# Performance work log

Measured on AMD Instinct MI355X. Metric: run time of the kernel, lower is better.

## Reference

```python
import jax, jax.numpy as jnp
import numpy as np

VOCAB, DIM, LAYERS, HEADS, FF, SEQ, BATCH = 32000, 1024, 4, 16, 4096, 2048, 2
HD = DIM // HEADS
EPS = 1e-6
ROPE_BASE = 10000.0


def setup_inputs() -> dict:
    key = jax.random.key(0)
    ks = jax.random.split(key, 10)
    std = 0.02
    return {
        "input_ids": jax.random.randint(ks[0], (BATCH, SEQ), 0, VOCAB, dtype=jnp.int32),
        "emb": jax.random.normal(ks[1], (VOCAB, DIM), jnp.float32) * std,
        "qkv_w": jax.random.normal(ks[2], (LAYERS, 3 * DIM, DIM), jnp.float32) * std,
        "out_w": jax.random.normal(ks[3], (LAYERS, DIM, DIM), jnp.float32) * std,
        "fc1_w": jax.random.normal(ks[4], (LAYERS, FF, DIM), jnp.float32) * std,
        "fc2_w": jax.random.normal(ks[5], (LAYERS, DIM, FF), jnp.float32) * std,
        "norm1_s": jnp.ones((LAYERS, DIM), jnp.float32),
        "norm2_s": jnp.ones((LAYERS, DIM), jnp.float32),
        "normf_s": jnp.ones((DIM,), jnp.float32),
        "lm_w": jax.random.normal(ks[6], (VOCAB, DIM), jnp.float32) * std,
    }


def _rms(x, scale):
    return x * jax.lax.rsqrt(jnp.mean(x * x, axis=-1, keepdims=True) + EPS) * scale


def _rope_tables(seq_len):
    inv_freq = 1.0 / (ROPE_BASE ** (jnp.arange(0, HD, 2, dtype=jnp.float32) / HD))
    freqs = jnp.arange(seq_len, dtype=jnp.float32)[:, None] * inv_freq[None, :]  # [S, HD/2]
    emb = jnp.concatenate([freqs, freqs], axis=-1)  # [S, HD]
    return jnp.cos(emb), jnp.sin(emb)


def _rotate_half(x):
    x1, x2 = jnp.split(x, 2, axis=-1)
    return jnp.concatenate([-x2, x1], axis=-1)


def _attention(h, qkv_w, out_w, cos, sin, mask):
    B, S, _ = h.shape
    qkv = jnp.einsum('bsd,ed->bse', h, qkv_w)  # [B, S, 3*DIM]
    qkv = qkv.reshape(B, S, 3, HEADS, HD).transpose(2, 0, 3, 1, 4)  # [3, B, H, S, hd]
    q, k, v = qkv[0], qkv[1], qkv[2]
    q = q * cos + _rotate_half(q) * sin
    k = k * cos + _rotate_half(k) * sin
    scores = jnp.einsum('bhqd,bhkd->bhqk', q, k) * (HD ** -0.5)
    scores = jnp.where(mask, scores, -jnp.inf)
    attn = jax.nn.softmax(scores, axis=-1)
    out = jnp.einsum('bhqk,bhkd->bhqd', attn, v)
    out = out.transpose(0, 2, 1, 3).reshape(B, S, DIM)
    return jnp.einsum('bsd,ed->bse', out, out_w)


def reference(input_ids, emb, qkv_w, out_w, fc1_w, fc2_w, norm1_s, norm2_s, normf_s, lm_w):
    B, S = input_ids.shape
    x = emb[input_ids]  # [B, S, DIM]
    cos, sin = _rope_tables(S)
    mask = jnp.tril(jnp.ones((S, S), dtype=bool))  # causal
    for l in range(LAYERS):
        x = x + _attention(_rms(x, norm1_s[l]), qkv_w[l], out_w[l], cos, sin, mask)
        h = _rms(x, norm2_s[l])
        ff = jnp.einsum('bsf,df->bsd', jax.nn.silu(jnp.einsum('bsd,fd->bsf', h, fc1_w[l])), fc2_w[l])
        x = x + ff
    logits = jnp.einsum('bsd,vd->bsv', _rms(x, normf_s), lm_w)
    return logits
```

## Files before the change

kernel.cpp:

```cpp
#include <hip/hip_runtime.h>

using u16 = unsigned short;
using u32 = unsigned int;
using bf16x8 = __attribute__((ext_vector_type(8))) __bf16;
using u16x8  = __attribute__((ext_vector_type(8))) u16;
using f32x4  = __attribute__((ext_vector_type(4))) float;
using u32x4  = __attribute__((ext_vector_type(4))) u32;

#define SEQ    2048
#define BATCH  2
#define DIM    1024
#define HEADS  16
#define HD     64
#define FF     4096
#define LAYERS 4
#define VOCAB  32000
#define ROWS   (BATCH*SEQ)

__device__ __forceinline__ u16 f2bf(float f) {
  u32 u = __float_as_uint(f);
  u += 0x7fffu + ((u >> 16) & 1u);
  return (u16)(u >> 16);
}
__device__ __forceinline__ float bf2f(u16 h) { return __uint_as_float(((u32)h) << 16); }

__device__ __forceinline__ void gload_lds16(const u16* g, u16* l) {
  __builtin_amdgcn_global_load_lds(
      (__attribute__((address_space(1))) void*)(u16*)g,
      (__attribute__((address_space(3))) void*)l, 16, 0, 0);
}

constexpr int BM = 128, BN = 128, BK = 32;

template<int EPI>
__global__ __launch_bounds__(256)
void gemm_nt(const u16* __restrict__ A, const u16* __restrict__ Bw,
             float* __restrict__ Cf, u16* __restrict__ Cb,
             int M, int N, int K)
{
  __shared__ __align__(16) u16 As[2][BM*BK];
  __shared__ __align__(16) u16 Bs[2][BN*BK];
  const int tid  = threadIdx.x;
  const int wid  = tid >> 6;
  const int lane = tid & 63;
  const int bn = blockIdx.x, bm = blockIdx.y;
  const int wm = wid >> 1, wn = wid & 1;

  f32x4 acc[4][4] = {};

  const int lr = lane >> 2;
  const int lk = (lane & 3) * 8;
  const u16* Ag0 = A  + (size_t)(bm*BM + wid*16     + lr)*K + lk;
  const u16* Ag1 = A  + (size_t)(bm*BM + (wid+4)*16 + lr)*K + lk;
  const u16* Bg0 = Bw + (size_t)(bn*BN + wid*16     + lr)*K + lk;
  const u16* Bg1 = Bw + (size_t)(bn*BN + (wid+4)*16 + lr)*K + lk;

  auto STG = [&](int buf, int k0) {
    gload_lds16(Ag0 + k0, &As[buf][ wid   *512]);
    gload_lds16(Ag1 + k0, &As[buf][(wid+4)*512]);
    gload_lds16(Bg0 + k0, &Bs[buf][ wid   *512]);
    gload_lds16(Bg1 + k0, &Bs[buf][(wid+4)*512]);
  };

  const int aoff = (wm*64 + (lane & 15))*BK + (lane >> 4)*8;
  const int boff = (wn*64 + (lane & 15))*BK + (lane >> 4)*8;

  STG(0, 0);
  const int nt = K / BK;
  for (int t = 0; t < nt; ++t) {
    __syncthreads();
    if (t + 1 < nt) STG((t+1) & 1, (t+1)*BK);
    const u16* Asf = &As[t & 1][aoff];
    const u16* Bsf = &Bs[t & 1][boff];
    bf16x8 af[4], bfr[4];
    #pragma unroll
    for (int m = 0; m < 4; ++m) af[m] = *(const bf16x8*)(Asf + m*16*BK);
    #pragma unroll
    for (int n = 0; n < 4; ++n) bfr[n] = *(const bf16x8*)(Bsf + n*16*BK);
    #pragma unroll
    for (int m = 0; m < 4; ++m)
      #pragma unroll
      for (int n = 0; n < 4; ++n)
        acc[m][n] = __builtin_amdgcn_mfma_f32_16x16x32_bf16(af[m], bfr[n], acc[m][n], 0, 0, 0);
  }

  const int row0 = bm*BM + wm*64 + (lane >> 4)*4;
  const int col0 = bn*BN + wn*64 + (lane & 15);
  #pragma unroll
  for (int m = 0; m < 4; ++m) {
    #pragma unroll
    for (int n = 0; n < 4; ++n) {
      #pragma unroll
      for (int r = 0; r < 4; ++r) {
        const size_t idx = (size_t)(row0 + m*16 + r)*N + (col0 + n*16);
        const float v = acc[m][n][r];
        if constexpr (EPI == 0)      Cf[idx] = v;
        else if constexpr (EPI == 1) Cf[idx] += v;
        else if constexpr (EPI == 2) Cb[idx] = f2bf(v / (1.f + __expf(-v)));
        else                         Cb[idx] = f2bf(v);
      }
    }
  }
}

#define GPHASE(buf, q, STAGE_STMT, WAITV)                                     \
  {                                                                           \
    if ((q) == 0) {                                                           \
      _Pragma("unroll") for (int n = 0; n < 4; ++n)                           \
        _Pragma("unroll") for (int ks = 0; ks < 2; ++ks)                      \
          bfrag[n][ks] = ldsB((buf), wn*64 + n*16, ks);                       \
    }                                                                         \
    bf16x8 afrag[2][2];                                                       \
    _Pragma("unroll") for (int mi = 0; mi < 2; ++mi)                          \
      _Pragma("unroll") for (int ks = 0; ks < 2; ++ks)                        \
        afrag[mi][ks] = ldsA((buf), wm*128 + (q)*32 + mi*16, ks);             \
    STAGE_STMT;                                                               \
    __builtin_amdgcn_s_barrier();                                             \
    asm volatile("" ::: "memory");                                            \
    __builtin_amdgcn_s_setprio(1);                                            \
    _Pragma("unroll") for (int mi = 0; mi < 2; ++mi)                          \
      _Pragma("unroll") for (int n = 0; n < 4; ++n)                           \
        _Pragma("unroll") for (int ks = 0; ks < 2; ++ks)                      \
          acc[(q)*2+mi][n] = __builtin_amdgcn_mfma_f32_16x16x32_bf16(         \
              afrag[mi][ks], bfrag[n][ks], acc[(q)*2+mi][n], 0, 0, 0);        \
    __builtin_amdgcn_s_setprio(0);                                            \
    if ((WAITV) == 1) asm volatile("s_waitcnt vmcnt(6)" ::: "memory");        \
    if ((WAITV) == 2) asm volatile("s_waitcnt vmcnt(0)" ::: "memory");        \
    __builtin_amdgcn_s_barrier();                                             \
    asm volatile("" ::: "memory");                                            \
  }

template<int EPI>
__global__ __launch_bounds__(512, 2)
void gemm_nt_256(const u16* __restrict__ A, const u16* __restrict__ Bw,
                 float* __restrict__ Cf, u16* __restrict__ Cb,
                 u16* __restrict__ qbo, u16* __restrict__ kbo,
                 u16* __restrict__ vto, const float* __restrict__ tab,
                 int M, int N, int K, int nbm)
{
  __shared__ __align__(16) u16 lds[2][2][256*64];
  const int tid = threadIdx.x, wid = tid >> 6, lane = tid & 63;
  const int nwg = gridDim.x;
  const int swz = (blockIdx.x & 7)*(nwg >> 3) + (blockIdx.x >> 3);
  const int bm = swz % nbm, bn = swz / nbm;
  const int wm = wid >> 2, wn = wid & 3;

  f32x4 acc[8][4] = {};

  const int lrow = lane >> 3;
  const int lkel = ((lane & 7) ^ lrow) * 8;
  const u16* Abase = A  + (size_t)(bm*256)*K + lkel;
  const u16* Bbase = Bw + (size_t)(bn*256)*K + lkel;
  auto stageA = [&](int buf, int ha, int t) {
    const int r0 = ha*64 + 8*wid, r1 = 128 + ha*64 + 8*wid;
    const size_t ko = (size_t)t*64;
    gload_lds16(Abase + (size_t)(r0 + lrow)*K + ko, &lds[buf][0][r0*64]);
    gload_lds16(Abase + (size_t)(r1 + lrow)*K + ko, &lds[buf][0][r1*64]);
  };
  auto stageB = [&](int buf, int hb, int t) {
    const int r0 = hb*128 + 8*wid, r1 = hb*128 + 64 + 8*wid;
    const size_t ko = (size_t)t*64;
    gload_lds16(Bbase + (size_t)(r0 + lrow)*K + ko, &lds[buf][1][r0*64]);
    gload_lds16(Bbase + (size_t)(r1 + lrow)*K + ko, &lds[buf][1][r1*64]);
  };

  const int frow = lane & 15, g = lane >> 4;
  auto ldsA = [&](int buf, int rowbase, int ks) -> bf16x8 {
    return *(const bf16x8*)&lds[buf][0][(rowbase + frow)*64 + ((ks*4 + g) ^ (lane & 7))*8];
  };
  auto ldsB = [&](int buf, int rowbase, int ks) -> bf16x8 {
    return *(const bf16x8*)&lds[buf][1][(rowbase + frow)*64 + ((ks*4 + g) ^ (lane & 7))*8];
  };

  bf16x8 bfrag[4][2];
  const int NT = K / 64;

  stageB(0,0,0); stageB(0,1,0); stageA(0,0,0); stageA(0,1,0);
  stageB(1,0,1); stageB(1,1,1); stageA(1,0,1);
  asm volatile("s_waitcnt vmcnt(6)" ::: "memory");
  __builtin_amdgcn_s_barrier();
  asm volatile("" ::: "memory");

  for (int i = 0; i < NT/2 - 1; ++i) {
    const int t0 = 2*i;
    GPHASE(0, 0, stageA(1,1,t0+1), 0)
    GPHASE(0, 1, stageB(0,0,t0+2), 0)
    GPHASE(0, 2, stageB(0,1,t0+2), 0)
    GPHASE(0, 3, stageA(0,0,t0+2), 1)
    GPHASE(1, 0, stageA(0,1,t0+2), 0)
    GPHASE(1, 1, stageB(1,0,t0+3), 0)
    GPHASE(1, 2, stageB(1,1,t0+3), 0)
    GPHASE(1, 3, stageA(1,0,t0+3), 1)
  }
  GPHASE(0, 0, stageA(1,1,NT-1), 0)
  GPHASE(0, 1, ((void)0), 0)
  GPHASE(0, 2, ((void)0), 0)
  GPHASE(0, 3, ((void)0), 2)
  GPHASE(1, 0, ((void)0), 0)
  GPHASE(1, 1, ((void)0), 0)
  GPHASE(1, 2, ((void)0), 0)
  GPHASE(1, 3, ((void)0), 0)

  if constexpr (EPI == 4) {
    const int hc = bn*4 + wn;
    const int which = hc >> 4, h = hc & 15;
    const int brow0 = bm*256 + wm*128 + g*4;
    const int b = brow0 >> 11;
    const int bh = b*HEADS + h;
    if (which == 2) {
      #pragma unroll
      for (int mrep = 0; mrep < 8; ++mrep) {
        const int s = (brow0 + mrep*16) & (SEQ-1);
        #pragma unroll
        for (int n = 0; n < 4; ++n) {
          const int d = frow + n*16;
          ushort4 pk;
          pk.x = f2bf(acc[mrep][n][0]); pk.y = f2bf(acc[mrep][n][1]);
          pk.z = f2bf(acc[mrep][n][2]); pk.w = f2bf(acc[mrep][n][3]);
          *(ushort4*)&vto[((size_t)bh*64 + d)*SEQ + s] = pk;
        }
      }
    } else {
      u16* outb = (which == 0) ? qbo : kbo;
      const float qs = (which == 0) ? 0.125f : 1.f;
      #pragma unroll
      for (int mrep = 0; mrep < 8; ++mrep) {
        #pragma unroll
        for (int rr = 0; rr < 4; ++rr) {
          const int s = (brow0 + mrep*16 + rr) & (SEQ-1);
          const float c0 = tab[s*64 + frow],      s0v = tab[s*64 + 32 + frow];
          const float c1 = tab[s*64 + 16 + frow], s1v = tab[s*64 + 48 + frow];
          const float x0 = acc[mrep][0][rr], x1 = acc[mrep][1][rr];
          const float x2 = acc[mrep][2][rr], x3 = acc[mrep][3][rr];
          u16* orow = outb + ((size_t)bh*SEQ + s)*64;
          orow[frow]      = f2bf((x0*c0 - x2*s0v)*qs);
          orow[frow + 32] = f2bf((x2*c0 + x0*s0v)*qs);
          orow[frow + 16] = f2bf((x1*c1 - x3*s1v)*qs);
          orow[frow + 48] = f2bf((x3*c1 + x1*s1v)*qs);
        }
      }
    }
  } else {
    const int row0 = bm*256 + wm*128 + g*4;
    const int col0 = bn*256 + wn*64 + frow;
    #pragma unroll
    for (int mrep = 0; mrep < 8; ++mrep) {
      #pragma unroll
      for (int n = 0; n < 4; ++n) {
        #pragma unroll
        for (int r = 0; r < 4; ++r) {
          const size_t idx = (size_t)(row0 + mrep*16 + r)*N + (col0 + n*16);
          const float v = acc[mrep][n][r];
          if constexpr (EPI == 0)      Cf[idx] = v;
          else if constexpr (EPI == 2) Cb[idx] = f2bf(v / (1.f + __expf(-v)));
        }
      }
    }
  }
}

__global__ void cvt_f32_bf16(const float* __restrict__ in, u16* __restrict__ out, int n4)
{
  const int i = blockIdx.x*256 + threadIdx.x;
  if (i >= n4) return;
  const float4 v = ((const float4*)in)[i];
  ushort4 o;
  o.x = f2bf(v.x); o.y = f2bf(v.y); o.z = f2bf(v.z); o.w = f2bf(v.w);
  ((ushort4*)out)[i] = o;
}

__global__ void embed_gather(const int* __restrict__ ids, const float* __restrict__ emb,
                             float* __restrict__ x)
{
  const int row = blockIdx.x, t = threadIdx.x;
  const int id = ids[row];
  ((float4*)(x + (size_t)row*DIM))[t] = ((const float4*)(emb + (size_t)id*DIM))[t];
}

__global__ __launch_bounds__(256)
void rmsnorm_bf16(const float* __restrict__ x, const float* __restrict__ scale,
                  u16* __restrict__ out)
{
  const int row = blockIdx.x, t = threadIdx.x;
  const float4 v = ((const float4*)(x + (size_t)row*DIM))[t];
  float ss = v.x*v.x + v.y*v.y + v.z*v.z + v.w*v.w;
  #pragma unroll
  for (int off = 32; off; off >>= 1) ss += __shfl_xor(ss, off);
  __shared__ float red[4];
  if ((t & 63) == 0) red[t >> 6] = ss;
  __syncthreads();
  const float tot = red[0] + red[1] + red[2] + red[3];
  const float r = rsqrtf(tot * (1.f/(float)DIM) + 1e-6f);
  const float4 sc = ((const float4*)scale)[t];
  ushort4 o;
  o.x = f2bf(v.x * r * sc.x);
  o.y = f2bf(v.y * r * sc.y);
  o.z = f2bf(v.z * r * sc.z);
  o.w = f2bf(v.w * r * sc.w);
  ((ushort4*)(out + (size_t)row*DIM))[t] = o;
}

__global__ void rope_table(float* __restrict__ tab)
{
  const int idx = blockIdx.x*256 + threadIdx.x;
  const int s = idx >> 5, i = idx & 31;
  const float invf = powf(10000.f, -(float)i/32.f);
  const float f = (float)s * invf;
  tab[s*64 + i]      = cosf(f);
  tab[s*64 + 32 + i] = sinf(f);
}

__global__ __launch_bounds__(256)
void attn_fwd(const u16* __restrict__ qb, const u16* __restrict__ kb,
              const u16* __restrict__ vt, u16* __restrict__ ctx)
{
  const int wid = threadIdx.x >> 6, lane = threadIdx.x & 63;
  const int bh = blockIdx.x >> 5, j = blockIdx.x & 31;
  const int qt = (wid == 0) ? j : (wid == 1) ? 63 - j : (wid == 2) ? 64 + j : 127 - j;
  const int q0 = qt * 16;
  const int g = lane >> 4, c15 = lane & 15;

  const u16* qbase = qb + (size_t)bh*SEQ*64;
  const u16* kbase = kb + (size_t)bh*SEQ*64;
  const u16* vtb   = vt + (size_t)bh*64*SEQ;

  const bf16x8 bQ0 = *(const bf16x8*)(qbase + (size_t)(q0 + c15)*64 + g*8);
  const bf16x8 bQ1 = *(const bf16x8*)(qbase + (size_t)(q0 + c15)*64 + 32 + g*8);

  f32x4 o[4] = {};
  float m = -INFINITY, lsum = 0.f;
  const int q_abs = q0 + c15;
  const int nt = (q0 >> 5) + 1;

  for (int t = 0; t < nt; ++t) {
    const int k0 = t*32;
    const u16* kr0 = kbase + (size_t)(k0 + c15)*64 + g*8;
    const u16* kr1 = kbase + (size_t)(k0 + 16 + c15)*64 + g*8;
    const bf16x8 aK00 = *(const bf16x8*)(kr0);
    const bf16x8 aK01 = *(const bf16x8*)(kr0 + 32);
    const bf16x8 aK10 = *(const bf16x8*)(kr1);
    const bf16x8 aK11 = *(const bf16x8*)(kr1 + 32);
    const f32x4 z = {};
    f32x4 sc0 = __builtin_amdgcn_mfma_f32_16x16x32_bf16(aK00, bQ0, z, 0,0,0);
    sc0 = __builtin_amdgcn_mfma_f32_16x16x32_bf16(aK01, bQ1, sc0, 0,0,0);
    f32x4 sc1 = __builtin_amdgcn_mfma_f32_16x16x32_bf16(aK10, bQ0, z, 0,0,0);
    sc1 = __builtin_amdgcn_mfma_f32_16x16x32_bf16(aK11, bQ1, sc1, 0,0,0);

    float s0[4], s1[4];
    if (k0 + 31 > q0) {
      #pragma unroll
      for (int r = 0; r < 4; ++r) {
        s0[r] = (k0 + 4*g + r      > q_abs) ? -INFINITY : sc0[r];
        s1[r] = (k0 + 16 + 4*g + r > q_abs) ? -INFINITY : sc1[r];
      }
    } else {
      #pragma unroll
      for (int r = 0; r < 4; ++r) { s0[r] = sc0[r]; s1[r] = sc1[r]; }
    }

    float tm = fmaxf(fmaxf(fmaxf(s0[0], s0[1]), fmaxf(s0[2], s0[3])),
                     fmaxf(fmaxf(s1[0], s1[1]), fmaxf(s1[2], s1[3])));
    tm = fmaxf(tm, __shfl_xor(tm, 16));
    tm = fmaxf(tm, __shfl_xor(tm, 32));

    if (!__all(tm <= m + 8.f)) {
      const float mnew = fmaxf(m, tm);
      const float corr = __expf(m - mnew);
      lsum *= corr;
      float corrq[4];
      #pragma unroll
      for (int r = 0; r < 4; ++r) corrq[r] = __shfl(corr, 4*g + r);
      #pragma unroll
      for (int dh = 0; dh < 4; ++dh)
        #pragma unroll
        for (int r = 0; r < 4; ++r) o[dh][r] *= corrq[r];
      m = mnew;
    }

    float p0[4], p1[4];
    #pragma unroll
    for (int r = 0; r < 4; ++r) { p0[r] = __expf(s0[r] - m); p1[r] = __expf(s1[r] - m); }
    float ps = (p0[0]+p0[1]) + (p0[2]+p0[3]) + (p1[0]+p1[1]) + (p1[2]+p1[3]);
    ps += __shfl_xor(ps, 16);
    ps += __shfl_xor(ps, 32);
    lsum += ps;

    u32 pk00, pk01, pk10, pk11;
    asm("v_cvt_pk_bf16_f32 %0, %1, %2" : "=v"(pk00) : "v"(p0[0]), "v"(p0[1]));
    asm("v_cvt_pk_bf16_f32 %0, %1, %2" : "=v"(pk01) : "v"(p0[2]), "v"(p0[3]));
    asm("v_cvt_pk_bf16_f32 %0, %1, %2" : "=v"(pk10) : "v"(p1[0]), "v"(p1[1]));
    asm("v_cvt_pk_bf16_f32 %0, %1, %2" : "=v"(pk11) : "v"(p1[2]), "v"(p1[3]));
    u32 w[4];
    #pragma unroll
    for (int wi = 0; wi < 4; ++wi) {
      const int src = c15 | ((((g << 1) + (wi >> 1)) & 3) << 4);
      const u32 a0 = __shfl((wi & 1) ? pk01 : pk00, src);
      const u32 a1 = __shfl((wi & 1) ? pk11 : pk10, src);
      w[wi] = (g < 2) ? a0 : a1;
    }
    const bf16x8 aP = __builtin_bit_cast(bf16x8, (u32x4){w[0], w[1], w[2], w[3]});

    #pragma unroll
    for (int dh = 0; dh < 4; ++dh) {
      const bf16x8 bV = *(const bf16x8*)(vtb + (size_t)(dh*16 + c15)*SEQ + k0 + g*8);
      o[dh] = __builtin_amdgcn_mfma_f32_16x16x32_bf16(aP, bV, o[dh], 0,0,0);
    }
  }

  float linv[4];
  #pragma unroll
  for (int r = 0; r < 4; ++r) linv[r] = 1.f / __shfl(lsum, 4*g + r);
  const int b = bh >> 4, h = bh & 15;
  #pragma unroll
  for (int r = 0; r < 4; ++r) {
    u16* crow = ctx + ((size_t)(b*SEQ + q0 + 4*g + r))*DIM + h*HD + c15;
    #pragma unroll
    for (int dh = 0; dh < 4; ++dh) crow[dh*16] = f2bf(o[dh][r] * linv[r]);
  }
}

extern "C" void kernel_launch(void* const* d_in, const int* in_sizes, int n_in,
                              void* d_out, int out_size, void* d_ws, size_t ws_size,
                              hipStream_t stream)
{
  const int*   ids   = (const int*)  d_in[0];
  const float* emb   = (const float*)d_in[1];
  const float* qkv_w = (const float*)d_in[2];
  const float* out_w = (const float*)d_in[3];
  const float* fc1_w = (const float*)d_in[4];
  const float* fc2_w = (const float*)d_in[5];
  const float* n1    = (const float*)d_in[6];
  const float* n2    = (const float*)d_in[7];
  const float* nf    = (const float*)d_in[8];
  const float* lm_w  = (const float*)d_in[9];
  float* logits = (float*)d_out;

  char* ws = (char*)d_ws;
  size_t off = 0;
  auto walloc = [&](size_t bytes) -> void* {
    void* p = ws + off;
    off += (bytes + 255) & ~(size_t)255;
    return p;
  };
  float* x     = (float*)walloc((size_t)ROWS*DIM*4);
  u16*   hbf   = (u16*)  walloc((size_t)ROWS*DIM*2);
  u16*   ctxbf = (u16*)  walloc((size_t)ROWS*DIM*2);
  u16*   gbf   = (u16*)  walloc((size_t)ROWS*FF*2);
  u16*   wq    = (u16*)  walloc((size_t)3*DIM*DIM*2);
  u16*   wo    = (u16*)  walloc((size_t)DIM*DIM*2);
  u16*   w1    = (u16*)  walloc((size_t)FF*DIM*2);
  u16*   w2    = (u16*)  walloc((size_t)DIM*FF*2);
  float* tab   = (float*)walloc((size_t)SEQ*64*4);
  u16* qbuf = (u16*)gbf;
  u16* kbuf = qbuf + (size_t)ROWS*DIM;
  u16* vtbuf= kbuf + (size_t)ROWS*DIM;
  u16* wlm = (u16*)ctxbf;

  rope_table<<<SEQ*32/256, 256, 0, stream>>>(tab);
  embed_gather<<<ROWS, 256, 0, stream>>>(ids, emb, x);

  for (int l = 0; l < LAYERS; ++l) {
    cvt_f32_bf16<<<3*DIM*DIM/4/256, 256, 0, stream>>>(qkv_w + (size_t)l*3*DIM*DIM, wq, 3*DIM*DIM/4);
    cvt_f32_bf16<<<DIM*DIM/4/256,   256, 0, stream>>>(out_w + (size_t)l*DIM*DIM,   wo, DIM*DIM/4);
    cvt_f32_bf16<<<FF*DIM/4/256,    256, 0, stream>>>(fc1_w + (size_t)l*FF*DIM,    w1, FF*DIM/4);
    cvt_f32_bf16<<<DIM*FF/4/256,    256, 0, stream>>>(fc2_w + (size_t)l*DIM*FF,    w2, DIM*FF/4);

    rmsnorm_bf16<<<ROWS, 256, 0, stream>>>(x, n1 + l*DIM, hbf);
    gemm_nt_256<4><<<(3*DIM/256)*(ROWS/256), 512, 0, stream>>>(
        hbf, wq, nullptr, nullptr, qbuf, kbuf, vtbuf, tab, ROWS, 3*DIM, DIM, ROWS/256);
    attn_fwd<<<BATCH*HEADS*(SEQ/64), 256, 0, stream>>>(qbuf, kbuf, vtbuf, ctxbf);
    gemm_nt<1><<<dim3(DIM/BN, ROWS/BM), 256, 0, stream>>>(ctxbf, wo, x, nullptr, ROWS, DIM, DIM);

    rmsnorm_bf16<<<ROWS, 256, 0, stream>>>(x, n2 + l*DIM, hbf);
    gemm_nt_256<2><<<(FF/256)*(ROWS/256), 512, 0, stream>>>(
        hbf, w1, nullptr, gbf, nullptr, nullptr, nullptr, nullptr, ROWS, FF, DIM, ROWS/256);
    gemm_nt<1><<<dim3(DIM/BN, ROWS/BM), 256, 0, stream>>>(gbf, w2, x, nullptr, ROWS, DIM, FF);
  }

  rmsnorm_bf16<<<ROWS, 256, 0, stream>>>(x, nf, hbf);
  cvt_f32_bf16<<<VOCAB*DIM/4/256, 256, 0, stream>>>(lm_w, wlm, VOCAB*DIM/4);
  gemm_nt_256<0><<<(VOCAB/256)*(ROWS/256), 512, 0, stream>>>(
      hbf, wlm, logits, nullptr, nullptr, nullptr, nullptr, nullptr, ROWS, VOCAB, DIM, ROWS/256);
}
```

Before: 1.792 ms.

## Split attention KV loop across wave pairs and merge partials via LDS

The attention kernel now gives each 16-row query tile to two waves. Each wave processes half of the causal key tiles, and the two partial softmax states are merged through shared memory using max/sum rescaling. This doubles the grid size to raise parallelism and shorten the longest per-wave serial KV loop. It costs a __syncthreads, an LDS round trip and idle half-waves at the end. Separately, the logits GEMM now uses nontemporal stores, and the inline-asm bf16 pack is replaced by software rounding, which adds ALU work.

```diff
diff --git a/kernel.cpp b/kernel.cpp
--- a/kernel.cpp
+++ b/kernel.cpp
@@ -251,8 +251,10 @@
         for (int r = 0; r < 4; ++r) {
           const size_t idx = (size_t)(row0 + mrep*16 + r)*N + (col0 + n*16);
           const float v = acc[mrep][n][r];
-          if constexpr (EPI == 0)      Cf[idx] = v;
-          else if constexpr (EPI == 2) Cb[idx] = f2bf(v / (1.f + __expf(-v)));
+          if constexpr (EPI == 0)
+            __builtin_nontemporal_store(v, &Cf[idx]);
+          else if constexpr (EPI == 2)
+            Cb[idx] = f2bf(v / (1.f + __expf(-v)));
         }
       }
     }
@@ -314,9 +316,11 @@
 void attn_fwd(const u16* __restrict__ qb, const u16* __restrict__ kb,
               const u16* __restrict__ vt, u16* __restrict__ ctx)
 {
+  __shared__ float st[4][64][18];
   const int wid = threadIdx.x >> 6, lane = threadIdx.x & 63;
-  const int bh = blockIdx.x >> 5, j = blockIdx.x & 31;
-  const int qt = (wid == 0) ? j : (wid == 1) ? 63 - j : (wid == 2) ? 64 + j : 127 - j;
+  const int bh = blockIdx.x >> 6, j = blockIdx.x & 63;
+  const int qt   = (wid < 2) ? j : 127 - j;
+  const int half = wid & 1;
   const int q0 = qt * 16;
   const int g = lane >> 4, c15 = lane & 15;
 
@@ -331,8 +335,11 @@
   float m = -INFINITY, lsum = 0.f;
   const int q_abs = q0 + c15;
   const int nt = (q0 >> 5) + 1;
-
-  for (int t = 0; t < nt; ++t) {
+  const int split = (nt + 1) >> 1;
+  const int tlo = half ? split : 0;
+  const int thi = half ? nt : split;
+
+  for (int t = tlo; t < thi; ++t) {
     const int k0 = t*32;
     const u16* kr0 = kbase + (size_t)(k0 + c15)*64 + g*8;
     const u16* kr1 = kbase + (size_t)(k0 + 16 + c15)*64 + g*8;
@@ -385,11 +392,10 @@
     ps += __shfl_xor(ps, 32);
     lsum += ps;
 
-    u32 pk00, pk01, pk10, pk11;
-    asm("v_cvt_pk_bf16_f32 %0, %1, %2" : "=v"(pk00) : "v"(p0[0]), "v"(p0[1]));
-    asm("v_cvt_pk_bf16_f32 %0, %1, %2" : "=v"(pk01) : "v"(p0[2]), "v"(p0[3]));
-    asm("v_cvt_pk_bf16_f32 %0, %1, %2" : "=v"(pk10) : "v"(p1[0]), "v"(p1[1]));
-    asm("v_cvt_pk_bf16_f32 %0, %1, %2" : "=v"(pk11) : "v"(p1[2]), "v"(p1[3]));
+    const u32 pk00 = (u32)f2bf(p0[0]) | ((u32)f2bf(p0[1]) << 16);
+    const u32 pk01 = (u32)f2bf(p0[2]) | ((u32)f2bf(p0[3]) << 16);
+    const u32 pk10 = (u32)f2bf(p1[0]) | ((u32)f2bf(p1[1]) << 16);
+    const u32 pk11 = (u32)f2bf(p1[2]) | ((u32)f2bf(p1[3]) << 16);
     u32 w[4];
     #pragma unroll
     for (int wi = 0; wi < 4; ++wi) {
@@ -407,15 +413,39 @@
     }
   }
 
-  float linv[4];
   #pragma unroll
-  for (int r = 0; r < 4; ++r) linv[r] = 1.f / __shfl(lsum, 4*g + r);
+  for (int dh = 0; dh < 4; ++dh)
+    #pragma unroll
+    for (int r = 0; r < 4; ++r) st[wid][lane][dh*4 + r] = o[dh][r];
+  st[wid][lane][16] = m;
+  st[wid][lane][17] = lsum;
+  __syncthreads();
+  if (half) return;
+
+  const float mB = st[wid+1][lane][16];
+  const float lB = st[wid+1][lane][17];
+  const float mS = fmaxf(m, mB);
+  const float cA = __expf(m - mS);
+  const float cB = __expf(mB - mS);
+  const float lS = lsum*cA + lB*cB;
+
+  float cAq[4], cBq[4], lSq[4];
+  #pragma unroll
+  for (int r = 0; r < 4; ++r) {
+    cAq[r] = __shfl(cA, 4*g + r);
+    cBq[r] = __shfl(cB, 4*g + r);
+    lSq[r] = __shfl(lS, 4*g + r);
+  }
   const int b = bh >> 4, h = bh & 15;
   #pragma unroll
   for (int r = 0; r < 4; ++r) {
     u16* crow = ctx + ((size_t)(b*SEQ + q0 + 4*g + r))*DIM + h*HD + c15;
-    #pragma unroll
-    for (int dh = 0; dh < 4; ++dh) crow[dh*16] = f2bf(o[dh][r] * linv[r]);
+    const float linv = 1.f / lSq[r];
+    #pragma unroll
+    for (int dh = 0; dh < 4; ++dh) {
+      const float om = o[dh][r]*cAq[r] + st[wid+1][lane][dh*4 + r]*cBq[r];
+      crow[dh*16] = f2bf(om * linv);
+    }
   }
 }
 
@@ -468,7 +498,7 @@
     rmsnorm_bf16<<<ROWS, 256, 0, stream>>>(x, n1 + l*DIM, hbf);
     gemm_nt_256<4><<<(3*DIM/256)*(ROWS/256), 512, 0, stream>>>(
         hbf, wq, nullptr, nullptr, qbuf, kbuf, vtbuf, tab, ROWS, 3*DIM, DIM, ROWS/256);
-    attn_fwd<<<BATCH*HEADS*(SEQ/64), 256, 0, stream>>>(qbuf, kbuf, vtbuf, ctxbf);
+    attn_fwd<<<BATCH*HEADS*(SEQ/32), 256, 0, stream>>>(qbuf, kbuf, vtbuf, ctxbf);
     gemm_nt<1><<<dim3(DIM/BN, ROWS/BM), 256, 0, stream>>>(ctxbf, wo, x, nullptr, ROWS, DIM, DIM);
 
     rmsnorm_bf16<<<ROWS, 256, 0, stream>>>(x, n2 + l*DIM, hbf);
```

Result: no change. 1.817 ms (+1.4%).
